# Kernel optimization log

Measured on AMD Instinct MI355X. Metric: run time of the kernel, lower is better.

Reference implementation:

```python
import jax, jax.numpy as jnp
import numpy as np

B, C, D, H, W = 2, 64, 8, 32, 32
QK = max(1, C // 8)  # intermediate dim for query/key 1x1x1 convs


def setup_inputs() -> dict:
    key = jax.random.key(0)
    ks = jax.random.split(key, 8)
    s = 0.05
    return {
        "x": jax.random.normal(ks[0], (B, C, D, H, W), dtype=jnp.float32),
        "Wq": jax.random.normal(ks[1], (QK, C), dtype=jnp.float32) * s,
        "bq": jax.random.normal(ks[2], (QK,), dtype=jnp.float32) * s,
        "Wk": jax.random.normal(ks[3], (QK, C), dtype=jnp.float32) * s,
        "bk": jax.random.normal(ks[4], (QK,), dtype=jnp.float32) * s,
        "Wv": jax.random.normal(ks[5], (C, C), dtype=jnp.float32) * s,
        "bv": jax.random.normal(ks[6], (C,), dtype=jnp.float32) * s,
        "gamma": jax.random.normal(ks[7], (1,), dtype=jnp.float32) * s,
    }


def reference(x, Wq, bq, Wk, bk, Wv, bv, gamma):
    b, c, d, h, w = x.shape
    n = d * h * w
    xf = x.reshape(b, c, n)  # (B, C, N)
    # 1x1x1 convs == per-position linear maps over channels
    q = jnp.einsum('oc,bcn->bon', Wq, xf) + bq[None, :, None]  # (B, QK, N)
    k = jnp.einsum('oc,bcn->bon', Wk, xf) + bk[None, :, None]  # (B, QK, N)
    v = jnp.einsum('oc,bcn->bon', Wv, xf) + bv[None, :, None]  # (B, C,  N)
    # energy[b, i, j] = q[b, :, i] . k[b, :, j]
    energy = jnp.einsum('bqi,bqj->bij', q, k)  # (B, N, N)
    attn = jax.nn.softmax(energy, axis=-1)
    # out[b, c, i] = sum_j v[b, c, j] * attn[b, i, j]
    out = jnp.einsum('bcj,bij->bci', v, attn)  # (B, C, N)
    out = out.reshape(b, c, d, h, w)
    return gamma[0] * out + x
```

## Files before the change

kernel.cpp:

```cpp
#include <hip/hip_runtime.h>


using f32x16 = __attribute__((ext_vector_type(16))) float;
using u32x4  = __attribute__((ext_vector_type(4))) unsigned int;
using bf16x8 = __attribute__((ext_vector_type(8))) short;

#define LOG2E 1.4426950408889634f

static __device__ __forceinline__ f32x16 mfma_z(u32x4 a, u32x4 b) {
  f32x16 z;
  #pragma unroll
  for (int r = 0; r < 16; ++r) z[r] = 0.f;
  return __builtin_amdgcn_mfma_f32_32x32x16_bf16(
      __builtin_bit_cast(bf16x8, a), __builtin_bit_cast(bf16x8, b), z, 0, 0, 0);
}
static __device__ __forceinline__ void mfma_acc(f32x16& d, u32x4 a, u32x4 b) {
  d = __builtin_amdgcn_mfma_f32_32x32x16_bf16(
      __builtin_bit_cast(bf16x8, a), __builtin_bit_cast(bf16x8, b), d, 0, 0, 0);
}
static __device__ __forceinline__ unsigned pkbf(float lo, float hi) {
  unsigned r;
  asm("v_cvt_pk_bf16_f32 %0, %1, %2" : "=v"(r) : "v"(lo), "v"(hi));
  return r;
}
static __device__ __forceinline__ void plswap(unsigned& a, unsigned& b) {
  asm("v_permlane32_swap_b32 %0, %1" : "+v"(a), "+v"(b));
}
static __device__ __forceinline__ float exp2_hw(float x) {
  return __builtin_amdgcn_exp2f(x);
}
static __device__ __forceinline__ unsigned f2bf(float f) {
  union { float f; unsigned u; } v; v.f = f;
  return (v.u + 0x7fffu + ((v.u >> 16) & 1u)) >> 16;
}
static __device__ __forceinline__ u32x4 pack8(const float* p) {
  u32x4 r;
  r[0] = f2bf(p[0]) | (f2bf(p[1]) << 16);
  r[1] = f2bf(p[2]) | (f2bf(p[3]) << 16);
  r[2] = f2bf(p[4]) | (f2bf(p[5]) << 16);
  r[3] = f2bf(p[6]) | (f2bf(p[7]) << 16);
  return r;
}

__global__ __launch_bounds__(128) void k_proj(
    const float* __restrict__ x,
    const float* __restrict__ Wq, const float* __restrict__ bq,
    const float* __restrict__ Wk, const float* __restrict__ bk,
    const float* __restrict__ Wv, const float* __restrict__ bv,
    u32x4* __restrict__ Qf, u32x4* __restrict__ Kf, u32x4* __restrict__ Vf) {
  __shared__ float sW[2][8][64];
  __shared__ float sb[2][8];
  __shared__ float sWv[4][64];
  __shared__ float sbv[4];
  const int tid = threadIdx.x;
  if (blockIdx.x < 256) {
    {
      float* wp = &sW[0][0][0];
      for (int i = tid; i < 512; i += 128) { wp[i] = Wq[i]; wp[512 + i] = Wk[i]; }
      if (tid < 8) { sb[0][tid] = bq[tid]; sb[1][tid] = bk[tid]; }
    }
    __syncthreads();
    const int b    = blockIdx.x >> 7;
    const int nb   = blockIdx.x & 127;
    const int lane = tid & 63;
    const int wv   = tid >> 6;
    const int ql   = lane & 31, ch = lane >> 5;
    const int n    = nb * 64 + wv * 32 + ql;
    const float* xp = x + ((size_t)b << 19) + n;
    float aq[8], ak[8];
    #pragma unroll
    for (int o = 0; o < 8; ++o) { aq[o] = 0.f; ak[o] = 0.f; }
    #pragma unroll
    for (int ci = 0; ci < 32; ci += 4) {
      const int c = ch * 32 + ci;
      float xv[4];
      #pragma unroll
      for (int j = 0; j < 4; ++j) xv[j] = xp[(size_t)(c + j) << 13];
      #pragma unroll
      for (int o = 0; o < 8; ++o) {
        const float4 wq = *(const float4*)&sW[0][o][c];
        const float4 wk = *(const float4*)&sW[1][o][c];
        aq[o] += wq.x * xv[0] + wq.y * xv[1] + wq.z * xv[2] + wq.w * xv[3];
        ak[o] += wk.x * xv[0] + wk.y * xv[1] + wk.z * xv[2] + wk.w * xv[3];
      }
    }
    #pragma unroll
    for (int o = 0; o < 8; ++o) {
      aq[o] += __shfl_xor(aq[o], 32, 64);
      ak[o] += __shfl_xor(ak[o], 32, 64);
    }
    if (ch == 0) {
      float q8[8], k8[8];
      #pragma unroll
      for (int o = 0; o < 8; ++o) {
        q8[o] = (aq[o] + sb[0][o]) * LOG2E;
        k8[o] = ak[o] + sb[1][o];
      }
      Qf[((size_t)b << 13) + n] = pack8(q8);
      Kf[((size_t)b << 13) + n] = pack8(k8);
    }
  } else {
    const int bid = blockIdx.x - 256;
    const int b   = bid >> 7;
    const int coq = (bid >> 3) & 15;
    const int ngc = bid & 7;
    const int ng  = ngc * 128 + tid;
    const int co  = coq * 4;
    for (int i = tid; i < 256; i += 128)
      sWv[i >> 6][i & 63] = Wv[(co + (i >> 6)) * 64 + (i & 63)];
    if (tid < 4) sbv[tid] = bv[co + tid];
    __syncthreads();
    float acc[4][8];
    #pragma unroll
    for (int i = 0; i < 4; ++i)
      #pragma unroll
      for (int e = 0; e < 8; ++e) acc[i][e] = 0.f;
    const float* xb = x + ((size_t)b << 19) + ((size_t)ng << 3);
    #pragma unroll 4
    for (int c = 0; c < 64; ++c) {
      const float4* xp = (const float4*)(xb + ((size_t)c << 13));
      const float4 x0 = xp[0];
      const float4 x1 = xp[1];
      #pragma unroll
      for (int i = 0; i < 4; ++i) {
        const float wv = sWv[i][c];
        acc[i][0] += wv * x0.x; acc[i][1] += wv * x0.y;
        acc[i][2] += wv * x0.z; acc[i][3] += wv * x0.w;
        acc[i][4] += wv * x1.x; acc[i][5] += wv * x1.y;
        acc[i][6] += wv * x1.z; acc[i][7] += wv * x1.w;
      }
    }
    #pragma unroll
    for (int i = 0; i < 4; ++i) {
      const int c = co + i;
      const float bias = sbv[i];
      float v8[8];
      #pragma unroll
      for (int e = 0; e < 8; ++e) v8[e] = acc[i][e] + bias;
      const int idx = ((b * 512 + (ng >> 1)) * 2 + (c >> 5)) * 64 + (ng & 1) * 32 + (c & 31);
      Vf[idx] = pack8(v8);
    }
  }
}

__global__ __launch_bounds__(512, 2) void k_attn(
    const u32x4* __restrict__ Qf, const u32x4* __restrict__ Kf, const u32x4* __restrict__ Vf,
    const float* __restrict__ x, const float* __restrict__ gamma, float* __restrict__ out) {
  __shared__ float sO[64][65];
  __shared__ float sl[64];
  const int tid  = threadIdx.x;
  const int b    = blockIdx.x >> 7;
  const int qb   = blockIdx.x & 127;
  const int i0   = qb * 64;
  const int w    = tid >> 6;
  const int lane = tid & 63;
  const int ql   = lane & 31;
  const int h    = lane >> 5;

  for (int i = tid; i < 64 * 65; i += 512) (&sO[0][0])[i] = 0.f;
  if (tid < 64) sl[tid] = 0.f;
  __syncthreads();

  u32x4 zer; zer[0] = 0u; zer[1] = 0u; zer[2] = 0u; zer[3] = 0u;
  const int qkbase = b * 8192;
  const u32x4 qf0 = (lane < 32) ? Qf[qkbase + i0 + lane] : zer;
  const u32x4 qf1 = (lane < 32) ? Qf[qkbase + i0 + 32 + lane] : zer;

  f32x16 acc00, acc01, acc10, acc11;
  #pragma unroll
  for (int r = 0; r < 16; ++r) { acc00[r] = 0.f; acc01[r] = 0.f; acc10[r] = 0.f; acc11[r] = 0.f; }
  float lacc0 = 0.f, lacc1 = 0.f;

  const int jbase = qkbase + w * 1024;
  const u32x4* __restrict__ vbase = Vf + ((size_t)(b * 512 + w * 64) << 7) + lane;

  auto tile = [&](const u32x4& kf, const u32x4* vf, const u32x4& qf,
                  f32x16& a0, f32x16& a1, float& lac) {
    f32x16 sacc = mfma_z(kf, qf);
    float p[16];
    #pragma unroll
    for (int r = 0; r < 16; ++r) p[r] = exp2_hw(sacc[r]);
    lac += (((p[0] + p[1]) + (p[2] + p[3])) + ((p[4] + p[5]) + (p[6] + p[7])))
         + (((p[8] + p[9]) + (p[10] + p[11])) + ((p[12] + p[13]) + (p[14] + p[15])));
    unsigned wd[4][2];
    #pragma unroll
    for (int qq = 0; qq < 4; ++qq) {
      wd[qq][0] = pkbf(p[4 * qq + 0], p[4 * qq + 1]);
      wd[qq][1] = pkbf(p[4 * qq + 2], p[4 * qq + 3]);
    }
    plswap(wd[0][0], wd[1][0]);
    plswap(wd[0][1], wd[1][1]);
    plswap(wd[2][0], wd[3][0]);
    plswap(wd[2][1], wd[3][1]);
    u32x4 pf0, pf1;
    pf0[0] = wd[0][0]; pf0[1] = wd[0][1]; pf0[2] = wd[1][0]; pf0[3] = wd[1][1];
    pf1[0] = wd[2][0]; pf1[1] = wd[2][1]; pf1[2] = wd[3][0]; pf1[3] = wd[3][1];
    mfma_acc(a0, vf[0], pf0);
    mfma_acc(a1, vf[1], pf0);
    mfma_acc(a0, vf[2], pf1);
    mfma_acc(a1, vf[3], pf1);
  };
  auto body = [&](const u32x4& kf, const u32x4* vf) {
    tile(kf, vf, qf0, acc00, acc01, lacc0);
    tile(kf, vf, qf1, acc10, acc11, lacc1);
  };

  u32x4 kA, kB, vA[4], vB[4];
  kA = (lane < 32) ? Kf[jbase + lane] : zer;
  { const u32x4* vp = vbase;
    vA[0] = vp[0]; vA[1] = vp[64]; vA[2] = vp[128]; vA[3] = vp[192]; }
  #pragma unroll 1
  for (int it = 0; it < 32; it += 2) {
    kB = (lane < 32) ? Kf[jbase + (it + 1) * 32 + lane] : zer;
    { const u32x4* vp = vbase + (size_t)(it + 1) * 256;
      vB[0] = vp[0]; vB[1] = vp[64]; vB[2] = vp[128]; vB[3] = vp[192]; }
    body(kA, vA);
    const int n2 = (it + 2) & 31;
    kA = (lane < 32) ? Kf[jbase + n2 * 32 + lane] : zer;
    { const u32x4* vp = vbase + (size_t)n2 * 256;
      vA[0] = vp[0]; vA[1] = vp[64]; vA[2] = vp[128]; vA[3] = vp[192]; }
    body(kB, vB);
  }

  #pragma unroll
  for (int r = 0; r < 16; ++r) {
    const int cr = (r & 3) + 8 * (r >> 2) + 4 * h;
    atomicAdd(&sO[cr][ql], acc00[r]);
    atomicAdd(&sO[cr + 32][ql], acc01[r]);
    atomicAdd(&sO[cr][32 + ql], acc10[r]);
    atomicAdd(&sO[cr + 32][32 + ql], acc11[r]);
  }
  atomicAdd(&sl[ql], lacc0);
  atomicAdd(&sl[32 + ql], lacc1);
  __syncthreads();

  const float g  = gamma[0];
  const int   c  = tid >> 3;
  const int   qg = (tid & 7) * 8;
  const size_t base = (((size_t)b * 64 + c) << 13) + i0 + qg;
  #pragma unroll
  for (int half = 0; half < 2; ++half) {
    const int q4 = qg + half * 4;
    const float4 xv = *(const float4*)&x[base + half * 4];
    float4 o;
    o.x = g * (sO[c][q4 + 0] / sl[q4 + 0]) + xv.x;
    o.y = g * (sO[c][q4 + 1] / sl[q4 + 1]) + xv.y;
    o.z = g * (sO[c][q4 + 2] / sl[q4 + 2]) + xv.z;
    o.w = g * (sO[c][q4 + 3] / sl[q4 + 3]) + xv.w;
    *(float4*)&out[base + half * 4] = o;
  }
}

extern "C" void kernel_launch(void* const* d_in, const int* in_sizes, int n_in,
                              void* d_out, int out_size, void* d_ws, size_t ws_size,
                              hipStream_t stream) {
  const float* x  = (const float*)d_in[0];
  const float* Wq = (const float*)d_in[1];
  const float* bq = (const float*)d_in[2];
  const float* Wk = (const float*)d_in[3];
  const float* bk = (const float*)d_in[4];
  const float* Wv = (const float*)d_in[5];
  const float* bv = (const float*)d_in[6];
  const float* gm = (const float*)d_in[7];
  if (ws_size < 2621440u) return;
  char* ws = (char*)d_ws;
  u32x4* Qf = (u32x4*)(ws);
  u32x4* Kf = (u32x4*)(ws + (256 << 10));
  u32x4* Vf = (u32x4*)(ws + (512 << 10));
  float* out = (float*)d_out;

  k_proj<<<dim3(512), dim3(128), 0, stream>>>(x, Wq, bq, Wk, bk, Wv, bv, Qf, Kf, Vf);
  k_attn<<<dim3(256), dim3(512), 0, stream>>>(Qf, Kf, Vf, x, gm, out);
}
```

Measured before the change: 79.52 us.

## Split attention key range across two blocks and combine partials in new kernel

After: 127.8 us. 60.7% more time.

```diff
diff --git a/kernel.cpp b/kernel.cpp
--- a/kernel.cpp
+++ b/kernel.cpp
@@ -6,6 +6,9 @@
 using bf16x8 = __attribute__((ext_vector_type(8))) short;
 
 #define LOG2E 1.4426950408889634f
+#define WS_BASE   2621440u
+#define SLOT_F    4160
+#define WS_SPLIT  (WS_BASE + 512u * SLOT_F * 4u)
 
 static __device__ __forceinline__ f32x16 mfma_z(u32x4 a, u32x4 b) {
   f32x16 z;
@@ -145,17 +148,20 @@
 
 __global__ __launch_bounds__(512, 2) void k_attn(
     const u32x4* __restrict__ Qf, const u32x4* __restrict__ Kf, const u32x4* __restrict__ Vf,
-    const float* __restrict__ x, const float* __restrict__ gamma, float* __restrict__ out) {
+    const float* __restrict__ x, const float* __restrict__ gamma, float* __restrict__ out,
+    float* __restrict__ pO, int split) {
   __shared__ float sO[64][65];
   __shared__ float sl[64];
   const int tid  = threadIdx.x;
-  const int b    = blockIdx.x >> 7;
-  const int qb   = blockIdx.x & 127;
+  int b, qb, s;
+  if (split) { b = blockIdx.x >> 8; qb = (blockIdx.x >> 1) & 127; s = blockIdx.x & 1; }
+  else       { b = blockIdx.x >> 7; qb = blockIdx.x & 127;        s = 0; }
   const int i0   = qb * 64;
   const int w    = tid >> 6;
   const int lane = tid & 63;
   const int ql   = lane & 31;
   const int h    = lane >> 5;
+  const int iters = split ? 16 : 32;
 
   for (int i = tid; i < 64 * 65; i += 512) (&sO[0][0])[i] = 0.f;
   if (tid < 64) sl[tid] = 0.f;
@@ -171,8 +177,9 @@
   for (int r = 0; r < 16; ++r) { acc00[r] = 0.f; acc01[r] = 0.f; acc10[r] = 0.f; acc11[r] = 0.f; }
   float lacc0 = 0.f, lacc1 = 0.f;
 
-  const int jbase = qkbase + w * 1024;
-  const u32x4* __restrict__ vbase = Vf + ((size_t)(b * 512 + w * 64) << 7) + lane;
+  const int kofs  = s * 4096 + w * (split ? 512 : 1024);
+  const int jbase = qkbase + kofs;
+  const u32x4* __restrict__ vbase = Vf + ((size_t)(b * 512 + (kofs >> 4)) << 7) + lane;
 
   auto tile = [&](const u32x4& kf, const u32x4* vf, const u32x4& qf,
                   f32x16& a0, f32x16& a1, float& lac) {
@@ -210,12 +217,12 @@
   { const u32x4* vp = vbase;
     vA[0] = vp[0]; vA[1] = vp[64]; vA[2] = vp[128]; vA[3] = vp[192]; }
   #pragma unroll 1
-  for (int it = 0; it < 32; it += 2) {
+  for (int it = 0; it < iters; it += 2) {
     kB = (lane < 32) ? Kf[jbase + (it + 1) * 32 + lane] : zer;
     { const u32x4* vp = vbase + (size_t)(it + 1) * 256;
       vB[0] = vp[0]; vB[1] = vp[64]; vB[2] = vp[128]; vB[3] = vp[192]; }
     body(kA, vA);
-    const int n2 = (it + 2) & 31;
+    const int n2 = (it + 2) & (iters - 1);
     kA = (lane < 32) ? Kf[jbase + n2 * 32 + lane] : zer;
     { const u32x4* vp = vbase + (size_t)n2 * 256;
       vA[0] = vp[0]; vA[1] = vp[64]; vA[2] = vp[128]; vA[3] = vp[192]; }
@@ -234,20 +241,67 @@
   atomicAdd(&sl[32 + ql], lacc1);
   __syncthreads();
 
+  if (split) {
+    float* slot = pO + (size_t)blockIdx.x * SLOT_F;
+    const int c  = tid >> 3;
+    const int qg = (tid & 7) * 8;
+    #pragma unroll
+    for (int half = 0; half < 2; ++half) {
+      float4 o;
+      o.x = sO[c][qg + half * 4 + 0];
+      o.y = sO[c][qg + half * 4 + 1];
+      o.z = sO[c][qg + half * 4 + 2];
+      o.w = sO[c][qg + half * 4 + 3];
+      *(float4*)&slot[c * 64 + qg + half * 4] = o;
+    }
+    if (tid < 64) slot[4096 + tid] = sl[tid];
+  } else {
+    const float g  = gamma[0];
+    const int   c  = tid >> 3;
+    const int   qg = (tid & 7) * 8;
+    const size_t base = (((size_t)b * 64 + c) << 13) + i0 + qg;
+    #pragma unroll
+    for (int half = 0; half < 2; ++half) {
+      const int q4 = qg + half * 4;
+      const float4 xv = *(const float4*)&x[base + half * 4];
+      float4 o;
+      o.x = g * (sO[c][q4 + 0] / sl[q4 + 0]) + xv.x;
+      o.y = g * (sO[c][q4 + 1] / sl[q4 + 1]) + xv.y;
+      o.z = g * (sO[c][q4 + 2] / sl[q4 + 2]) + xv.z;
+      o.w = g * (sO[c][q4 + 3] / sl[q4 + 3]) + xv.w;
+      *(float4*)&out[base + half * 4] = o;
+    }
+  }
+}
+
+__global__ __launch_bounds__(256) void k_combine(
+    const float* __restrict__ pO, const float* __restrict__ x,
+    const float* __restrict__ gamma, float* __restrict__ out) {
+  __shared__ float sl[64];
+  const int tid = threadIdx.x;
+  const int b   = blockIdx.x >> 7;
+  const int qb  = blockIdx.x & 127;
+  const int i0  = qb * 64;
+  const float* s0 = pO + (size_t)(b * 256 + qb * 2) * SLOT_F;
+  const float* s1 = s0 + SLOT_F;
+  if (tid < 64) sl[tid] = s0[4096 + tid] + s1[4096 + tid];
+  __syncthreads();
   const float g  = gamma[0];
-  const int   c  = tid >> 3;
-  const int   qg = (tid & 7) * 8;
+  const int   c  = tid >> 2;
+  const int   qg = (tid & 3) * 16;
   const size_t base = (((size_t)b * 64 + c) << 13) + i0 + qg;
   #pragma unroll
-  for (int half = 0; half < 2; ++half) {
-    const int q4 = qg + half * 4;
-    const float4 xv = *(const float4*)&x[base + half * 4];
+  for (int v = 0; v < 4; ++v) {
+    const int q4 = qg + v * 4;
+    const float4 o0 = *(const float4*)&s0[c * 64 + q4];
+    const float4 o1 = *(const float4*)&s1[c * 64 + q4];
+    const float4 xv = *(const float4*)&x[base + v * 4];
     float4 o;
-    o.x = g * (sO[c][q4 + 0] / sl[q4 + 0]) + xv.x;
-    o.y = g * (sO[c][q4 + 1] / sl[q4 + 1]) + xv.y;
-    o.z = g * (sO[c][q4 + 2] / sl[q4 + 2]) + xv.z;
-    o.w = g * (sO[c][q4 + 3] / sl[q4 + 3]) + xv.w;
-    *(float4*)&out[base + half * 4] = o;
+    o.x = g * ((o0.x + o1.x) / sl[q4 + 0]) + xv.x;
+    o.y = g * ((o0.y + o1.y) / sl[q4 + 1]) + xv.y;
+    o.z = g * ((o0.z + o1.z) / sl[q4 + 2]) + xv.z;
+    o.w = g * ((o0.w + o1.w) / sl[q4 + 3]) + xv.w;
+    *(float4*)&out[base + v * 4] = o;
   }
 }
 
@@ -262,13 +316,17 @@
   const float* Wv = (const float*)d_in[5];
   const float* bv = (const float*)d_in[6];
   const float* gm = (const float*)d_in[7];
-  if (ws_size < 2621440u) return;
+  if (ws_size < WS_BASE) return;
+  const int split = (ws_size >= WS_SPLIT) ? 1 : 0;
   char* ws = (char*)d_ws;
   u32x4* Qf = (u32x4*)(ws);
   u32x4* Kf = (u32x4*)(ws + (256 << 10));
   u32x4* Vf = (u32x4*)(ws + (512 << 10));
+  float* pO = (float*)(ws + WS_BASE);
   float* out = (float*)d_out;
 
   k_proj<<<dim3(512), dim3(128), 0, stream>>>(x, Wq, bq, Wk, bk, Wv, bv, Qf, Kf, Vf);
-  k_attn<<<dim3(256), dim3(512), 0, stream>>>(Qf, Kf, Vf, x, gm, out);
-}
+  k_attn<<<dim3(split ? 512 : 256), dim3(512), 0, stream>>>(Qf, Kf, Vf, x, gm, out, pO, split);
+  if (split)
+    k_combine<<<dim3(256), dim3(256), 0, stream>>>(pO, x, gm, out);
+}
```
